# Kernel optimization log

Hardware: AMD Instinct MI355X
Metric: run time of the kernel (lower is better)

Reference implementation:

```python
import jax, jax.numpy as jnp
import numpy as np

B, S, D = 4, 2048, 1024
H = 16
DH = D // H  # 64
DFF = 4096
EPS = 1e-5


def _layer_norm(x, g, b):
    mu = jnp.mean(x, axis=-1, keepdims=True)
    var = jnp.mean((x - mu) ** 2, axis=-1, keepdims=True)
    return (x - mu) * jax.lax.rsqrt(var + EPS) * g + b


def _rope(x):
    # x: [B, S, H, DH]; same rotation for every head (module reuses one RoPE).
    inv_freq = 1.0 / (10000.0 ** (jnp.arange(0, DH, 2, dtype=jnp.float32) / DH))
    pos = jnp.arange(S, dtype=jnp.float32)
    freqs = pos[:, None] * inv_freq[None, :]            # [S, DH/2]
    cos = jnp.cos(freqs)[None, :, None, :]              # [1, S, 1, DH/2]
    sin = jnp.sin(freqs)[None, :, None, :]
    x_even = x[..., 0::2]
    x_odd = x[..., 1::2]
    r_even = x_even * cos - x_odd * sin
    r_odd = x_even * sin + x_odd * cos
    return jnp.stack([r_even, r_odd], axis=-1).reshape(x.shape)


def setup_inputs() -> dict:
    key = jax.random.key(0)
    ks = jax.random.split(key, 10)
    s_d = 1.0 / np.sqrt(D)
    s_f = 1.0 / np.sqrt(DFF)
    return {
        "x": jax.random.normal(ks[0], (B, S, D), jnp.float32),
        "Wq": jax.random.uniform(ks[1], (D, D), jnp.float32, -s_d, s_d),
        "bq": jnp.zeros((D,), jnp.float32),
        "Wk": jax.random.uniform(ks[2], (D, D), jnp.float32, -s_d, s_d),
        "bk": jnp.zeros((D,), jnp.float32),
        "Wv": jax.random.uniform(ks[3], (D, D), jnp.float32, -s_d, s_d),
        "bv": jnp.zeros((D,), jnp.float32),
        "Wo": jax.random.uniform(ks[4], (D, D), jnp.float32, -s_d, s_d),
        "bo": jnp.zeros((D,), jnp.float32),
        "W1": jax.random.uniform(ks[5], (DFF, D), jnp.float32, -s_d, s_d),
        "bf1": jnp.zeros((DFF,), jnp.float32),
        "W2": jax.random.uniform(ks[6], (D, DFF), jnp.float32, -s_f, s_f),
        "bf2": jnp.zeros((D,), jnp.float32),
        "g1": jnp.ones((D,), jnp.float32),
        "be1": jnp.zeros((D,), jnp.float32),
        "g2": jnp.ones((D,), jnp.float32),
        "be2": jnp.zeros((D,), jnp.float32),
    }


def reference(x, Wq, bq, Wk, bk, Wv, bv, Wo, bo, W1, bf1, W2, bf2, g1, be1, g2, be2):
    # Pre-LN self-attention block (dropout is identity at eval)
    residual = x
    h = _layer_norm(x, g1, be1)
    q = (h @ Wq.T + bq).reshape(B, S, H, DH)
    k = (h @ Wk.T + bk).reshape(B, S, H, DH)
    v = (h @ Wv.T + bv).reshape(B, S, H, DH)
    q = _rope(q)
    k = _rope(k)
    # scores: [B, H, Sq, Sk]
    scores = jnp.einsum("bqhd,bkhd->bhqk", q, k) / np.sqrt(DH)
    causal = jnp.tril(jnp.ones((S, S), dtype=bool))
    scores = jnp.where(causal[None, None], scores, -jnp.inf)
    attn = jax.nn.softmax(scores, axis=-1)
    out = jnp.einsum("bhqk,bkhd->bqhd", attn, v).reshape(B, S, D)
    out = out @ Wo.T + bo
    x = residual + out
    # FFN block
    residual = x
    h = _layer_norm(x, g2, be2)
    ff = jax.nn.relu(h @ W1.T + bf1) @ W2.T + bf2
    return residual + ff
```

## Files before the change

kernel.cpp:

```cpp
#include <hip/hip_runtime.h>

typedef __attribute__((ext_vector_type(8))) short bh8;
typedef __attribute__((ext_vector_type(4))) short sh4;
typedef __attribute__((ext_vector_type(4))) float f4;
typedef __attribute__((ext_vector_type(16))) float f16v;
typedef __attribute__((ext_vector_type(4))) unsigned int u4;

__device__ __forceinline__ unsigned short f2bf(float x) {
  unsigned int u = __float_as_uint(x);
  u += 0x7fffu + ((u >> 16) & 1u);
  return (unsigned short)(u >> 16);
}
__device__ __forceinline__ float bf2f(short x) {
  return __uint_as_float(((unsigned int)(unsigned short)x) << 16);
}
__device__ __forceinline__ unsigned cvtpk_bf16(float lo, float hi) {
  unsigned r;
  asm("v_cvt_pk_bf16_f32 %0, %1, %2" : "=v"(r) : "v"(lo), "v"(hi));
  return r;
}
__device__ __forceinline__ void gl_lds16(const short* g, short* l) {
  __builtin_amdgcn_global_load_lds(
      (const __attribute__((address_space(1))) unsigned int*)g,
      (__attribute__((address_space(3))) unsigned int*)l, 16, 0, 0);
}

#define VM2() asm volatile("s_waitcnt vmcnt(2)" ::: "memory")
#define VM0() asm volatile("s_waitcnt vmcnt(0)" ::: "memory")

__global__ __launch_bounds__(256)
void rope_table(float* __restrict__ ct, float* __restrict__ st) {
  const int idx = blockIdx.x * 256 + threadIdx.x;
  const int s = idx >> 5, j = idx & 31;
  const float invf = expf(-0.28782313662425574f * (float)j);
  const float f = (float)s * invf;
  ct[idx] = cosf(f);
  st[idx] = sinf(f);
}

__global__ __launch_bounds__(256)
void concat_bias(const float* __restrict__ bq, const float* __restrict__ bk,
                 const float* __restrict__ bv, float* __restrict__ bqkv) {
  const int i = blockIdx.x * 256 + threadIdx.x;
  bqkv[i] = (i < 1024) ? bq[i] : ((i < 2048) ? bk[i - 1024] : bv[i - 2048]);
}

__global__ __launch_bounds__(256)
void w2bf_all(const float* __restrict__ Wq, const float* __restrict__ Wk,
              const float* __restrict__ Wv, const float* __restrict__ Wo,
              const float* __restrict__ W1, const float* __restrict__ W2,
              short* __restrict__ wqkvb, short* __restrict__ wob,
              short* __restrict__ w1b, short* __restrict__ w2b) {
  const int which = blockIdx.y;
  const float* src; short* dst; int n;
  switch (which) {
    case 0: src = Wq; dst = wqkvb;                 n = 1 << 20; break;
    case 1: src = Wk; dst = wqkvb + (1 << 20);     n = 1 << 20; break;
    case 2: src = Wv; dst = wqkvb + (2 << 20);     n = 1 << 20; break;
    case 3: src = Wo; dst = wob;                   n = 1 << 20; break;
    case 4: src = W1; dst = w1b;                   n = 1 << 22; break;
    default: src = W2; dst = w2b;                  n = 1 << 22; break;
  }
  const int i = (blockIdx.x * 256 + threadIdx.x) * 4;
  if (i >= n) return;
  f4 v = *(const f4*)(src + i);
#pragma unroll
  for (int j = 0; j < 4; ++j) dst[i + j] = (short)f2bf(v[j]);
}

__global__ __launch_bounds__(256)
void layernorm_bf(const float* __restrict__ x, const float* __restrict__ g,
                  const float* __restrict__ be, short* __restrict__ out) {
  __shared__ float sb[4];
  const int row = blockIdx.x, t = threadIdx.x;
  const float* xr = x + (size_t)row * 1024;
  f4 v = *(const f4*)(xr + t * 4);
  float s = v[0] + v[1] + v[2] + v[3];
#pragma unroll
  for (int mk = 1; mk < 64; mk <<= 1) s += __shfl_xor(s, mk, 64);
  if ((t & 63) == 0) sb[t >> 6] = s;
  __syncthreads();
  const float mean = (sb[0] + sb[1] + sb[2] + sb[3]) * (1.0f / 1024.0f);
  __syncthreads();
  f4 d;
#pragma unroll
  for (int i = 0; i < 4; ++i) d[i] = v[i] - mean;
  float s2 = d[0] * d[0] + d[1] * d[1] + d[2] * d[2] + d[3] * d[3];
#pragma unroll
  for (int mk = 1; mk < 64; mk <<= 1) s2 += __shfl_xor(s2, mk, 64);
  if ((t & 63) == 0) sb[t >> 6] = s2;
  __syncthreads();
  const float var = (sb[0] + sb[1] + sb[2] + sb[3]) * (1.0f / 1024.0f);
  const float rstd = rsqrtf(var + 1e-5f);
  const f4 gg = *(const f4*)(g + t * 4);
  const f4 bb = *(const f4*)(be + t * 4);
#pragma unroll
  for (int i = 0; i < 4; ++i)
    out[(size_t)row * 1024 + t * 4 + i] = (short)f2bf(d[i] * rstd * gg[i] + bb[i]);
}

#define STG(dst, gbase, kt, half)                                              \
  {                                                                            \
    _Pragma("unroll") for (int cc = 0; cc < 2; ++cc) {                         \
      const int rr = (half) * 128 + cc * 64 + sr;                              \
      gl_lds16(gbase + (size_t)rr * K + (kt) * 64 + ssl * 8,                   \
               &dst[rr * 64 + (t & 7) * 8]);                                   \
    }                                                                          \
  }

#define PH64(bf, q, STAGE_STMT, VMSTMT)                                        \
  {                                                                            \
    if ((q) == 0) {                                                            \
      _Pragma("unroll") for (int ni = 0; ni < 2; ++ni)                         \
      _Pragma("unroll") for (int kk = 0; kk < 2; ++kk)                         \
        bfrag[ni][kk] = *(const bh8*)(&Bs[bf][(wn * 32 + ni * 16 + (lane & 15)) * 64 + (((lane >> 4) + kk * 4) ^ (lane & 7)) * 8]); \
    }                                                                          \
    _Pragma("unroll") for (int j = 0; j < 2; ++j)                              \
    _Pragma("unroll") for (int kk = 0; kk < 2; ++kk)                           \
      af[j][kk] = *(const bh8*)(&As[bf][(wm * 64 + (2 * (q) + j) * 16 + (lane & 15)) * 64 + (((lane >> 4) + kk * 4) ^ (lane & 7)) * 8]); \
    STAGE_STMT;                                                                \
    __builtin_amdgcn_s_barrier();                                              \
    asm volatile("s_waitcnt lgkmcnt(0)" ::: "memory");                         \
    __builtin_amdgcn_sched_barrier(0);                                         \
    __builtin_amdgcn_s_setprio(1);                                             \
    _Pragma("unroll") for (int j = 0; j < 2; ++j)                              \
    _Pragma("unroll") for (int ni = 0; ni < 2; ++ni)                           \
    _Pragma("unroll") for (int kk = 0; kk < 2; ++kk)                           \
      acc[2 * (q) + j][ni] = __builtin_amdgcn_mfma_f32_16x16x32_bf16(          \
          af[j][kk], bfrag[ni][kk], acc[2 * (q) + j][ni], 0, 0, 0);            \
    __builtin_amdgcn_s_setprio(0);                                             \
    VMSTMT;                                                                    \
    __builtin_amdgcn_s_barrier();                                              \
  }

template <int RELU, int RES, int OBF16, int QKVMODE>
__global__ __launch_bounds__(512, 4)
void gemm_bn128(const short* __restrict__ A, const short* __restrict__ Bw,
                const float* __restrict__ bias, const float* __restrict__ res,
                const float* __restrict__ ct, const float* __restrict__ st,
                short* __restrict__ Vt,
                short* __restrict__ Cb, float* __restrict__ Cf,
                int M, int N, int K) {
  __shared__ short As[2][128 * 64];
  __shared__ short Bs[2][128 * 64];
  const int t = threadIdx.x, lane = t & 63;
  const int w = t >> 6, wm = w >> 2, wn = w & 3;
  const int nwg = gridDim.x, cpx = nwg >> 3;
  int flat = blockIdx.x;
  flat = (flat & 7) * cpx + (flat >> 3);
  const int nbn = N >> 7;
  const int bn = flat % nbn, bm = flat / nbn;
  const short* Ab = A + (size_t)(bm * 128) * K;
  const short* Bb = Bw + (size_t)(bn * 128) * K;
  const int nkt = K >> 6;
  const int sr = t >> 3;
  const int ssl = (t & 7) ^ (sr & 7);
  f4 acc[4][2] = {};
  bh8 bfrag[2][2], af[2][2];

  STG(Bs[0], Bb, 0, 0); STG(As[0], Ab, 0, 0);
  STG(Bs[1], Bb, 1, 0);
  VM2();
  __builtin_amdgcn_s_barrier();

  for (int i2 = 0; i2 < nkt; i2 += 2) {
    const bool nf = (i2 + 2 < nkt);
    PH64(0, 0, STG(As[1], Ab, i2 + 1, 0), );
    PH64(0, 1, if (nf) STG(Bs[0], Bb, i2 + 2, 0),
         if (nf) { VM2(); } else { VM0(); });
    PH64(1, 0, if (nf) STG(As[0], Ab, i2 + 2, 0), );
    PH64(1, 1, if (nf) STG(Bs[1], Bb, i2 + 3, 0), if (nf) { VM2(); });
  }

  const int rb = bm * 128 + wm * 64 + ((lane >> 4) << 2);
  const int cb = bn * 128 + wn * 32 + (lane & 15);
  if (QKVMODE && bn >= 16) {
#pragma unroll
    for (int mi = 0; mi < 4; ++mi) {
#pragma unroll
      for (int ni = 0; ni < 2; ++ni) {
        const int c = cb + ni * 16;
        const float bi = bias[c];
        const int hh = (c - 2048) >> 6, dd = (c - 2048) & 63;
        const int r0 = rb + mi * 16;
        const int bb2 = r0 >> 11, ss = r0 & 2047;
        sh4 pk;
#pragma unroll
        for (int jr = 0; jr < 4; ++jr) pk[jr] = (short)f2bf(acc[mi][ni][jr] + bi);
        *(sh4*)(Vt + ((size_t)(bb2 * 16 + hh) * 64 + dd) * 2048 + ss) = pk;
      }
    }
  } else if (QKVMODE) {
    const bool evenc = (lane & 1) == 0;
#pragma unroll
    for (int mi = 0; mi < 4; ++mi) {
#pragma unroll
      for (int ni = 0; ni < 2; ++ni) {
        const int c = cb + ni * 16;
        const float bi = bias[c];
        const int j0 = (c & 63) >> 1;
#pragma unroll
        for (int jr = 0; jr < 4; ++jr) {
          const int r = rb + mi * 16 + jr;
          const int s = r & 2047;
          const float v = acc[mi][ni][jr] + bi;
          const float pv = __shfl_xor(v, 1, 64);
          const float cs = ct[s * 32 + j0], sn = st[s * 32 + j0];
          const float o = evenc ? (v * cs - pv * sn) : (pv * sn + v * cs);
          Cb[(size_t)r * N + c] = (short)f2bf(o);
        }
      }
    }
  } else {
#pragma unroll
    for (int mi = 0; mi < 4; ++mi) {
#pragma unroll
      for (int ni = 0; ni < 2; ++ni) {
        const int c = cb + ni * 16;
        const float bi = bias[c];
#pragma unroll
        for (int jr = 0; jr < 4; ++jr) {
          const int r = rb + mi * 16 + jr;
          float v = acc[mi][ni][jr] + bi;
          if (RES) v += res[(size_t)r * N + c];
          if (RELU) v = fmaxf(v, 0.f);
          if (OBF16) Cb[(size_t)r * N + c] = (short)f2bf(v);
          else       Cf[(size_t)r * N + c] = v;
        }
      }
    }
  }
}

__global__ __launch_bounds__(512, 4)
void flash_attn(const short* __restrict__ qkv, const short* __restrict__ vt,
                short* __restrict__ o) {
  __shared__ short lds[2 * 2 * 64 * 72];
  const int t = threadIdx.x, lane = t & 63, w = t >> 6;
  const int l31 = lane & 31, l5 = lane >> 5;
  const int id = blockIdx.x;
  const int half = id >> 8, j = id & 255;
  const int xcd = j & 7, y = j >> 3;
  const int bh = xcd * 8 + (y >> 2);
  const int pr = y & 3;
  const int qt = half ? pr : 7 - pr;
  const int b = bh >> 4, hh = bh & 15;
  const int r8 = t >> 3, c8 = (t & 7) * 8;
  const float NEG_INF = -__builtin_inff();

  const short* kbase = qkv + (size_t)b * 2048 * 3072 + 1024 + hh * 64;
  const short* vbase = vt + ((size_t)bh * 64 + r8) * 2048;
  const int wq0 = qt * 256 + w * 32;
  const int nt = 4 * qt + 4;

  bh8 qf[4];
  {
    const short* qrow = qkv + ((size_t)b * 2048 + wq0 + l31) * 3072 + hh * 64 + l5 * 8;
#pragma unroll
    for (int dk = 0; dk < 4; ++dk) qf[dk] = *(const bh8*)(qrow + dk * 16);
  }
  f16v o0 = {}, o1 = {};
  float mr = NEG_INF, lsum = 0.f;

  {
    bh8 rk = *(const bh8*)(kbase + (size_t)r8 * 3072 + c8);
    bh8 rv = *(const bh8*)(vbase + c8);
    *(bh8*)(&lds[r8 * 72 + c8]) = rk;
    *(bh8*)(&lds[4608 + r8 * 72 + c8]) = rv;
  }

  for (int kt = 0; kt < nt; ++kt) {
    __syncthreads();
    const int cur = kt & 1, nxt = cur ^ 1;
    bh8 rk, rv;
    const bool more = (kt + 1 < nt);
    if (more) {
      rk = *(const bh8*)(kbase + (size_t)((kt + 1) * 64 + r8) * 3072 + c8);
      rv = *(const bh8*)(vbase + (kt + 1) * 64 + c8);
    }
    const int kvb = kt * 64;
    if (kvb <= wq0 + 31) {
      const short* Kl = &lds[cur * 9216];
      const short* Vl = &lds[cur * 9216 + 4608];
      f16v s0 = {}, s1 = {};
#pragma unroll
      for (int dk = 0; dk < 4; ++dk) {
        bh8 ka0 = *(const bh8*)(&Kl[l31 * 72 + dk * 16 + l5 * 8]);
        bh8 ka1 = *(const bh8*)(&Kl[(32 + l31) * 72 + dk * 16 + l5 * 8]);
        s0 = __builtin_amdgcn_mfma_f32_32x32x16_bf16(ka0, qf[dk], s0, 0, 0, 0);
        s1 = __builtin_amdgcn_mfma_f32_32x32x16_bf16(ka1, qf[dk], s1, 0, 0, 0);
      }
      if (kvb + 63 > wq0) {
        const int qq = wq0 + l31;
        const int kvo = kvb + l5 * 4;
#pragma unroll
        for (int r = 0; r < 16; ++r) {
          const int kv0 = kvo + (r & 3) + 8 * (r >> 2);
          if (kv0 > qq) s0[r] = NEG_INF;
          if (kv0 + 32 > qq) s1[r] = NEG_INF;
        }
      }
      float mx = s0[0];
#pragma unroll
      for (int r = 1; r < 16; ++r) mx = fmaxf(mx, s0[r]);
#pragma unroll
      for (int r = 0; r < 16; ++r) mx = fmaxf(mx, s1[r]);
      mx = fmaxf(mx, __shfl_xor(mx, 32, 64));
      const bool keep = __all(mx <= mr + 8.0f);
      float mn, al;
      if (keep) { mn = mr; al = 1.0f; }
      else {
        mn = fmaxf(mr, mx);
        al = __expf((mr - mn) * 0.125f);
        mr = mn;
      }
      float rsA = 0.f, rsB = 0.f;
#pragma unroll
      for (int r = 0; r < 16; ++r) {
        const float p0 = __expf((s0[r] - mn) * 0.125f);
        const float p1 = __expf((s1[r] - mn) * 0.125f);
        s0[r] = p0; s1[r] = p1;
        rsA += p0; rsB += p1;
      }
      float rs = rsA + rsB;
      rs += __shfl_xor(rs, 32, 64);
      if (keep) {
        lsum += rs;
      } else {
        lsum = lsum * al + rs;
#pragma unroll
        for (int r = 0; r < 16; ++r) { o0[r] *= al; o1[r] *= al; }
      }
      float pp[32];
#pragma unroll
      for (int r = 0; r < 16; ++r) { pp[r] = s0[r]; pp[16 + r] = s1[r]; }
      const bool lo32 = (l5 == 0);
#pragma unroll
      for (int ks = 0; ks < 4; ++ks) {
        const int base = (ks >> 1) * 16 + (ks & 1) * 8;
        const unsigned e0 = cvtpk_bf16(pp[base + 0], pp[base + 1]);
        const unsigned e1 = cvtpk_bf16(pp[base + 2], pp[base + 3]);
        const unsigned q0 = cvtpk_bf16(pp[base + 4], pp[base + 5]);
        const unsigned q1 = cvtpk_bf16(pp[base + 6], pp[base + 7]);
        const unsigned sel0 = lo32 ? q0 : e0;
        const unsigned sel1 = lo32 ? q1 : e1;
        const unsigned rx0 = (unsigned)__shfl_xor((int)sel0, 32, 64);
        const unsigned rx1 = (unsigned)__shfl_xor((int)sel1, 32, 64);
        u4 frag;
        frag[0] = lo32 ? e0 : rx0;
        frag[1] = lo32 ? e1 : rx1;
        frag[2] = lo32 ? rx0 : q0;
        frag[3] = lo32 ? rx1 : q1;
        const bh8 pb = *(const bh8*)&frag;
        bh8 va0 = *(const bh8*)(&Vl[l31 * 72 + ks * 16 + l5 * 8]);
        bh8 va1 = *(const bh8*)(&Vl[(32 + l31) * 72 + ks * 16 + l5 * 8]);
        o0 = __builtin_amdgcn_mfma_f32_32x32x16_bf16(va0, pb, o0, 0, 0, 0);
        o1 = __builtin_amdgcn_mfma_f32_32x32x16_bf16(va1, pb, o1, 0, 0, 0);
      }
    }
    if (more) {
      *(bh8*)(&lds[nxt * 9216 + r8 * 72 + c8]) = rk;
      *(bh8*)(&lds[nxt * 9216 + 4608 + r8 * 72 + c8]) = rv;
    }
  }

  const float inv = 1.0f / lsum;
  __syncthreads();
  short* Ot = lds;
#pragma unroll
  for (int r = 0; r < 16; ++r) {
    const int d = (r & 3) + 8 * (r >> 2) + 4 * l5;
    Ot[(w * 32 + l31) * 72 + d]      = (short)f2bf(o0[r] * inv);
    Ot[(w * 32 + l31) * 72 + 32 + d] = (short)f2bf(o1[r] * inv);
  }
  __syncthreads();
  const int qrow = t >> 1, hf = t & 1;
  short* orow = o + ((size_t)b * 2048 + qt * 256 + qrow) * 1024 + hh * 64 + hf * 32;
#pragma unroll
  for (int i = 0; i < 4; ++i)
    *(bh8*)(orow + i * 8) = *(const bh8*)(&Ot[qrow * 72 + hf * 32 + i * 8]);
}

extern "C" void kernel_launch(void* const* d_in, const int* in_sizes, int n_in,
                              void* d_out, int out_size, void* d_ws, size_t ws_size,
                              hipStream_t stream) {
  const float* x   = (const float*)d_in[0];
  const float* Wq  = (const float*)d_in[1];
  const float* bq  = (const float*)d_in[2];
  const float* Wk  = (const float*)d_in[3];
  const float* bk  = (const float*)d_in[4];
  const float* Wv  = (const float*)d_in[5];
  const float* bv  = (const float*)d_in[6];
  const float* Wo  = (const float*)d_in[7];
  const float* bo  = (const float*)d_in[8];
  const float* W1  = (const float*)d_in[9];
  const float* bf1 = (const float*)d_in[10];
  const float* W2  = (const float*)d_in[11];
  const float* bf2 = (const float*)d_in[12];
  const float* g1  = (const float*)d_in[13];
  const float* be1 = (const float*)d_in[14];
  const float* g2  = (const float*)d_in[15];
  const float* be2 = (const float*)d_in[16];
  float* out = (float*)d_out;

  char* ws = (char*)d_ws;
  const size_t MB = 1u << 20;
  short* h_ob  = (short*)ws;
  short* qkv   = (short*)(ws + 16 * MB);
  short* f1    = (short*)(ws + 16 * MB);
  short* vtb   = (short*)(ws + 64 * MB);
  short* wqkvb = (short*)(ws + 80 * MB);
  short* wob   = (short*)(ws + 86 * MB);
  short* w1b   = (short*)(ws + 88 * MB);
  short* w2b   = (short*)(ws + 96 * MB);
  float* ct    = (float*)(ws + 104 * MB);
  float* st    = ct + 65536;
  float* bqkv  = st + 65536;
  float* x2    = out;

  rope_table<<<256, 256, 0, stream>>>(ct, st);
  concat_bias<<<12, 256, 0, stream>>>(bq, bk, bv, bqkv);
  w2bf_all<<<dim3(4096, 6), 256, 0, stream>>>(Wq, Wk, Wv, Wo, W1, W2,
                                              wqkvb, wob, w1b, w2b);

  layernorm_bf<<<8192, 256, 0, stream>>>(x, g1, be1, h_ob);

  gemm_bn128<0, 0, 1, 1><<<1536, 512, 0, stream>>>(h_ob, wqkvb, bqkv, nullptr,
                                                   ct, st, vtb, qkv, nullptr,
                                                   8192, 3072, 1024);

  flash_attn<<<512, 512, 0, stream>>>(qkv, vtb, h_ob);

  gemm_bn128<0, 1, 0, 0><<<512, 512, 0, stream>>>(h_ob, wob, bo, x,
                                                  nullptr, nullptr, nullptr,
                                                  nullptr, x2, 8192, 1024, 1024);

  layernorm_bf<<<8192, 256, 0, stream>>>(x2, g2, be2, h_ob);

  gemm_bn128<1, 0, 1, 0><<<2048, 512, 0, stream>>>(h_ob, w1b, bf1, nullptr,
                                                   nullptr, nullptr, nullptr,
                                                   f1, nullptr, 8192, 4096, 1024);

  gemm_bn128<0, 1, 0, 0><<<512, 512, 0, stream>>>(f1, w2b, bf2, x2,
                                                  nullptr, nullptr, nullptr,
                                                  nullptr, out, 8192, 1024, 4096);
}
```

Baseline: 360.1 us.

## Add 256x256 pipelined FFN1 GEMM, split attention tiles, fold softmax scale into Q

Replaces the FFN up-projection GEMM with a dedicated 256x256-tile kernel that has double-buffered LDS staging, swizzled fragments, barrier-phased MFMA and XCD-aware block remapping, aiming for higher operand reuse. Flash attention is reworked to 128-row query tiles with 256-thread blocks and twice as many blocks, for better load balance across CUs. The 1/sqrt(dh) scale moves into the QKV epilogue for Q, removing a multiply per exp in attention. These changes raise register pressure in the new GEMM and alter the rounding of Q.

```diff
diff --git a/kernel.cpp b/kernel.cpp
--- a/kernel.cpp
+++ b/kernel.cpp
@@ -25,6 +25,7 @@
       (__attribute__((address_space(3))) unsigned int*)l, 16, 0, 0);
 }
 
+#define VM4() asm volatile("s_waitcnt vmcnt(4)" ::: "memory")
 #define VM2() asm volatile("s_waitcnt vmcnt(2)" ::: "memory")
 #define VM0() asm volatile("s_waitcnt vmcnt(0)" ::: "memory")
 
@@ -192,6 +193,7 @@
     }
   } else if (QKVMODE) {
     const bool evenc = (lane & 1) == 0;
+    const float qsc = (bn < 8) ? 0.125f : 1.0f;
 #pragma unroll
     for (int mi = 0; mi < 4; ++mi) {
 #pragma unroll
@@ -206,7 +208,7 @@
           const float v = acc[mi][ni][jr] + bi;
           const float pv = __shfl_xor(v, 1, 64);
           const float cs = ct[s * 32 + j0], sn = st[s * 32 + j0];
-          const float o = evenc ? (v * cs - pv * sn) : (pv * sn + v * cs);
+          const float o = (evenc ? (v * cs - pv * sn) : (pv * sn + v * cs)) * qsc;
           Cb[(size_t)r * N + c] = (short)f2bf(o);
         }
       }
@@ -232,26 +234,108 @@
   }
 }
 
-__global__ __launch_bounds__(512, 4)
+#define PH256(bf, q, STAGE_STMT, VMSTMT)                                       \
+  {                                                                            \
+    if ((q) == 0) {                                                            \
+      _Pragma("unroll") for (int ni = 0; ni < 4; ++ni)                         \
+      _Pragma("unroll") for (int kk = 0; kk < 2; ++kk)                         \
+        bfrag[ni][kk] = *(const bh8*)(&Bs[bf][(wn * 64 + ni * 16 + (lane & 15)) * 64 + (((lane >> 4) + kk * 4) ^ (lane & 7)) * 8]); \
+    }                                                                          \
+    _Pragma("unroll") for (int j = 0; j < 2; ++j)                              \
+    _Pragma("unroll") for (int kk = 0; kk < 2; ++kk)                           \
+      af[j][kk] = *(const bh8*)(&As[bf][(wm * 128 + (2 * (q) + j) * 16 + (lane & 15)) * 64 + (((lane >> 4) + kk * 4) ^ (lane & 7)) * 8]); \
+    STAGE_STMT;                                                                \
+    __builtin_amdgcn_s_barrier();                                              \
+    asm volatile("s_waitcnt lgkmcnt(0)" ::: "memory");                         \
+    __builtin_amdgcn_sched_barrier(0);                                         \
+    __builtin_amdgcn_s_setprio(1);                                             \
+    _Pragma("unroll") for (int j = 0; j < 2; ++j)                              \
+    _Pragma("unroll") for (int ni = 0; ni < 4; ++ni)                           \
+    _Pragma("unroll") for (int kk = 0; kk < 2; ++kk)                           \
+      acc[2 * (q) + j][ni] = __builtin_amdgcn_mfma_f32_16x16x32_bf16(          \
+          af[j][kk], bfrag[ni][kk], acc[2 * (q) + j][ni], 0, 0, 0);            \
+    __builtin_amdgcn_s_setprio(0);                                             \
+    VMSTMT;                                                                    \
+    __builtin_amdgcn_s_barrier();                                              \
+  }
+
+__global__ __launch_bounds__(512, 2)
+void gemm256_ff1(const short* __restrict__ A, const short* __restrict__ Bw,
+                 const float* __restrict__ bias, short* __restrict__ Cb,
+                 int M, int N, int K) {
+  __shared__ short As[2][256 * 64];
+  __shared__ short Bs[2][256 * 64];
+  const int t = threadIdx.x, lane = t & 63;
+  const int w = t >> 6, wm = w >> 2, wn = w & 3;
+  const int nwg = gridDim.x, cpx = nwg >> 3;
+  int flat = blockIdx.x;
+  flat = (flat & 7) * cpx + (flat >> 3);
+  const int nbn = N >> 8;
+  const int bn = flat % nbn, bm = flat / nbn;
+  const short* Ab = A + (size_t)(bm * 256) * K;
+  const short* Bb = Bw + (size_t)(bn * 256) * K;
+  const int nkt = K >> 6;
+  const int sr = t >> 3;
+  const int ssl = (t & 7) ^ (sr & 7);
+  f4 acc[8][4] = {};
+  bh8 bfrag[4][2], af[2][2];
+
+  STG(Bs[0], Bb, 0, 0); STG(Bs[0], Bb, 0, 1);
+  STG(As[0], Ab, 0, 0); STG(As[0], Ab, 0, 1);
+  STG(Bs[1], Bb, 1, 0); STG(Bs[1], Bb, 1, 1);
+  VM4();
+  __builtin_amdgcn_s_barrier();
+
+  for (int i2 = 0; i2 < nkt; i2 += 2) {
+    const bool nf = (i2 + 2 < nkt);
+    PH256(0, 0, STG(As[1], Ab, i2 + 1, 0), );
+    PH256(0, 1, STG(As[1], Ab, i2 + 1, 1), );
+    PH256(0, 2, if (nf) STG(Bs[0], Bb, i2 + 2, 0), );
+    PH256(0, 3, if (nf) STG(Bs[0], Bb, i2 + 2, 1),
+          if (nf) { VM4(); } else { VM0(); });
+    PH256(1, 0, if (nf) STG(As[0], Ab, i2 + 2, 0), );
+    PH256(1, 1, if (nf) STG(As[0], Ab, i2 + 2, 1), );
+    PH256(1, 2, if (nf) STG(Bs[1], Bb, i2 + 3, 0), );
+    PH256(1, 3, if (nf) STG(Bs[1], Bb, i2 + 3, 1), if (nf) { VM4(); });
+  }
+
+  const int rb = bm * 256 + wm * 128 + ((lane >> 4) << 2);
+  const int cb = bn * 256 + wn * 64 + (lane & 15);
+#pragma unroll
+  for (int mi = 0; mi < 8; ++mi) {
+#pragma unroll
+    for (int ni = 0; ni < 4; ++ni) {
+      const int c = cb + ni * 16;
+      const float bi = bias[c];
+#pragma unroll
+      for (int jr = 0; jr < 4; ++jr) {
+        const int r = rb + mi * 16 + jr;
+        Cb[(size_t)r * N + c] = (short)f2bf(fmaxf(acc[mi][ni][jr] + bi, 0.f));
+      }
+    }
+  }
+}
+
+__global__ __launch_bounds__(256, 4)
 void flash_attn(const short* __restrict__ qkv, const short* __restrict__ vt,
                 short* __restrict__ o) {
   __shared__ short lds[2 * 2 * 64 * 72];
   const int t = threadIdx.x, lane = t & 63, w = t >> 6;
   const int l31 = lane & 31, l5 = lane >> 5;
   const int id = blockIdx.x;
-  const int half = id >> 8, j = id & 255;
+  const int half = id >> 9, j = id & 511;
   const int xcd = j & 7, y = j >> 3;
-  const int bh = xcd * 8 + (y >> 2);
-  const int pr = y & 3;
-  const int qt = half ? pr : 7 - pr;
+  const int bh = xcd * 8 + (y >> 3);
+  const int pr = y & 7;
+  const int qt = half ? pr : 15 - pr;
   const int b = bh >> 4, hh = bh & 15;
   const int r8 = t >> 3, c8 = (t & 7) * 8;
   const float NEG_INF = -__builtin_inff();
 
   const short* kbase = qkv + (size_t)b * 2048 * 3072 + 1024 + hh * 64;
-  const short* vbase = vt + ((size_t)bh * 64 + r8) * 2048;
-  const int wq0 = qt * 256 + w * 32;
-  const int nt = 4 * qt + 4;
+  const short* vbase = vt + (size_t)bh * 64 * 2048;
+  const int wq0 = qt * 128 + w * 32;
+  const int nt = 2 * qt + 2;
 
   bh8 qf[4];
   {
@@ -262,21 +346,28 @@
   f16v o0 = {}, o1 = {};
   float mr = NEG_INF, lsum = 0.f;
 
-  {
-    bh8 rk = *(const bh8*)(kbase + (size_t)r8 * 3072 + c8);
-    bh8 rv = *(const bh8*)(vbase + c8);
-    *(bh8*)(&lds[r8 * 72 + c8]) = rk;
-    *(bh8*)(&lds[4608 + r8 * 72 + c8]) = rv;
+  bh8 rk[2], rv[2];
+#pragma unroll
+  for (int p = 0; p < 2; ++p) {
+    rk[p] = *(const bh8*)(kbase + (size_t)(p * 32 + r8) * 3072 + c8);
+    rv[p] = *(const bh8*)(vbase + (size_t)(p * 32 + r8) * 2048 + c8);
+  }
+#pragma unroll
+  for (int p = 0; p < 2; ++p) {
+    *(bh8*)(&lds[(p * 32 + r8) * 72 + c8]) = rk[p];
+    *(bh8*)(&lds[4608 + (p * 32 + r8) * 72 + c8]) = rv[p];
   }
 
   for (int kt = 0; kt < nt; ++kt) {
     __syncthreads();
     const int cur = kt & 1, nxt = cur ^ 1;
-    bh8 rk, rv;
     const bool more = (kt + 1 < nt);
     if (more) {
-      rk = *(const bh8*)(kbase + (size_t)((kt + 1) * 64 + r8) * 3072 + c8);
-      rv = *(const bh8*)(vbase + (kt + 1) * 64 + c8);
+#pragma unroll
+      for (int p = 0; p < 2; ++p) {
+        rk[p] = *(const bh8*)(kbase + (size_t)((kt + 1) * 64 + p * 32 + r8) * 3072 + c8);
+        rv[p] = *(const bh8*)(vbase + (size_t)(p * 32 + r8) * 2048 + (kt + 1) * 64 + c8);
+      }
     }
     const int kvb = kt * 64;
     if (kvb <= wq0 + 31) {
@@ -311,14 +402,14 @@
       if (keep) { mn = mr; al = 1.0f; }
       else {
         mn = fmaxf(mr, mx);
-        al = __expf((mr - mn) * 0.125f);
+        al = __expf(mr - mn);
         mr = mn;
       }
       float rsA = 0.f, rsB = 0.f;
 #pragma unroll
       for (int r = 0; r < 16; ++r) {
-        const float p0 = __expf((s0[r] - mn) * 0.125f);
-        const float p1 = __expf((s1[r] - mn) * 0.125f);
+        const float p0 = __expf(s0[r] - mn);
+        const float p1 = __expf(s1[r] - mn);
         s0[r] = p0; s1[r] = p1;
         rsA += p0; rsB += p1;
       }
@@ -359,8 +450,11 @@
       }
     }
     if (more) {
-      *(bh8*)(&lds[nxt * 9216 + r8 * 72 + c8]) = rk;
-      *(bh8*)(&lds[nxt * 9216 + 4608 + r8 * 72 + c8]) = rv;
+#pragma unroll
+      for (int p = 0; p < 2; ++p) {
+        *(bh8*)(&lds[nxt * 9216 + (p * 32 + r8) * 72 + c8]) = rk[p];
+        *(bh8*)(&lds[nxt * 9216 + 4608 + (p * 32 + r8) * 72 + c8]) = rv[p];
+      }
     }
   }
 
@@ -375,7 +469,7 @@
   }
   __syncthreads();
   const int qrow = t >> 1, hf = t & 1;
-  short* orow = o + ((size_t)b * 2048 + qt * 256 + qrow) * 1024 + hh * 64 + hf * 32;
+  short* orow = o + ((size_t)b * 2048 + qt * 128 + qrow) * 1024 + hh * 64 + hf * 32;
 #pragma unroll
   for (int i = 0; i < 4; ++i)
     *(bh8*)(orow + i * 8) = *(const bh8*)(&Ot[qrow * 72 + hf * 32 + i * 8]);
@@ -429,7 +523,7 @@
                                                    ct, st, vtb, qkv, nullptr,
                                                    8192, 3072, 1024);
 
-  flash_attn<<<512, 512, 0, stream>>>(qkv, vtb, h_ob);
+  flash_attn<<<1024, 256, 0, stream>>>(qkv, vtb, h_ob);
 
   gemm_bn128<0, 1, 0, 0><<<512, 512, 0, stream>>>(h_ob, wob, bo, x,
                                                   nullptr, nullptr, nullptr,
@@ -437,9 +531,7 @@
 
   layernorm_bf<<<8192, 256, 0, stream>>>(x2, g2, be2, h_ob);
 
-  gemm_bn128<1, 0, 1, 0><<<2048, 512, 0, stream>>>(h_ob, w1b, bf1, nullptr,
-                                                   nullptr, nullptr, nullptr,
-                                                   f1, nullptr, 8192, 4096, 1024);
+  gemm256_ff1<<<512, 512, 0, stream>>>(h_ob, w1b, bf1, f1, 8192, 4096, 1024);
 
   gemm_bn128<0, 1, 0, 0><<<512, 512, 0, stream>>>(f1, w2b, bf2, x2,
                                                   nullptr, nullptr, nullptr,
```

After: 353.4 us. No clear change (-1.8%).
